# Optimization experiments

Hardware: AMD Instinct MI355X
Metric: run time of the kernel (lower is better)

The kernel has to match this reference:

```python
import jax, jax.numpy as jnp
import numpy as np

# Forest topology: T full C-ary trees of depth D, processed level-by-level
# (leaves=level 0 -> roots=level D), mirroring dgl.prop_nodes_topo.
T, C, D = 4096, 2, 5
E, H = 256, 128
COUNTS = [C ** (D - d) for d in range(D + 1)]          # nodes per level in one tree
OFFS = np.cumsum([0] + COUNTS[:-1])                     # level offsets within a tree
S = int(sum(COUNTS))                                    # nodes per tree (63)
N = T * S                                               # total nodes (258048)


def _topology():
    # children indices + validity mask for one tree, then tile across the forest
    ch1 = np.zeros((S, C), np.int32)
    m1 = np.zeros((S, C), np.float32)
    for d in range(1, D + 1):
        for j in range(COUNTS[d]):
            p = OFFS[d] + j
            ch1[p] = OFFS[d - 1] + j * C + np.arange(C)
            m1[p] = 1.0
    children = (ch1[None] + (np.arange(T, dtype=np.int32) * S)[:, None, None]).reshape(N, C)
    mask = np.tile(m1, (T, 1))
    return children, mask


def _level_nodes(d):
    # global node indices at level d (static numpy, not traced)
    return (np.arange(T)[:, None] * S + OFFS[d] + np.arange(COUNTS[d])[None, :]).reshape(-1)


def setup_inputs() -> dict:
    key = jax.random.key(0)
    ks = jax.random.split(key, 6)
    children, mask = _topology()
    child_type = np.asarray(jax.random.randint(ks[0], (N, C), 0, 2), np.int32)
    sc = 0.05
    return {
        "emb": jax.random.normal(ks[1], (N, E), jnp.float32),
        "child_mask": jnp.asarray(mask),
        "W_iou": jax.random.normal(ks[2], (E, 3 * H), jnp.float32) * sc,
        "U_iou": jax.random.normal(ks[3], (2 * H, 3 * H), jnp.float32) * sc,
        "b_iou": jnp.zeros((3 * H,), jnp.float32),
        "W_f": jax.random.normal(ks[4], (E, H), jnp.float32) * sc,
        "U_f_w": jax.random.normal(ks[5], (2 * H, 2 * H), jnp.float32) * sc,
        "U_f_b": jnp.zeros((2 * H,), jnp.float32),
        "b_f": jnp.zeros((H,), jnp.float32),
        "children_idx": jnp.asarray(children),
        "child_type": jnp.asarray(child_type),
    }


def _forward(emb, child_mask, W_iou, U_iou, b_iou, W_f, U_f_w, U_f_b, b_f,
             children_idx, child_type):
    h = jnp.zeros((N, H), emb.dtype)
    c = jnp.zeros((N, H), emb.dtype)
    for d in range(D + 1):  # topological sweep; leaves reduce to zeros (no children)
        nodes = _level_nodes(d)                          # [M] static
        ch = children_idx[nodes]                         # [M, C]
        cm = child_mask[nodes]                           # [M, C]
        ty = child_type[nodes]                           # [M, C]
        h_ch = h[ch]                                     # [M, C, H] mailbox gather
        c_ch = c[ch]
        # type-masked child-hidden sums (reduce_func)
        ht0 = jnp.einsum('mc,mch->mh', jnp.where(ty == 0, cm, 0.0), h_ch)
        ht1 = jnp.einsum('mc,mch->mh', jnp.where(ty == 1, cm, 0.0), h_ch)
        h_iou = jnp.concatenate([ht0, ht1], axis=1)      # [M, 2H]
        # per-child forget gates, selected by child type
        f = (h_iou @ U_f_w + U_f_b).reshape(-1, 2, H)
        idx = jnp.broadcast_to(ty[:, :, None], ty.shape + (H,))
        f_cell = jnp.take_along_axis(f, idx, axis=1)     # [M, C, H]
        X = emb[nodes] @ W_f                             # [M, H]
        f_tk = jax.nn.sigmoid(X[:, None, :] + f_cell + b_f)
        c_cell = jnp.sum(f_tk * c_ch * cm[:, :, None], axis=1)
        # apply_node_func
        iou = emb[nodes] @ W_iou + h_iou @ U_iou + b_iou
        i, o, u = jnp.split(iou, 3, axis=1)
        c_new = jax.nn.sigmoid(i) * jnp.tanh(u) + c_cell
        h_new = jax.nn.sigmoid(o) * jnp.tanh(c_new)
        h = h.at[nodes].set(h_new)
        c = c.at[nodes].set(c_new)
    return h


def reference(emb, child_mask, W_iou, U_iou, b_iou, W_f, U_f_w, U_f_b, b_f,
              children_idx, child_type):
    return _forward(emb, child_mask, W_iou, U_iou, b_iou, W_f, U_f_w, U_f_b, b_f,
                    children_idx, child_type)
```

## Files before the change

kernel.cpp:

```cpp
#include <hip/hip_runtime.h>


typedef float f32x4 __attribute__((ext_vector_type(4)));
typedef __bf16 bf16x8 __attribute__((ext_vector_type(8)));

__device__ __forceinline__ unsigned short f2bf(float x) {
  unsigned int u = __float_as_uint(x);
  return (unsigned short)((u + 0x7fffu + ((u >> 16) & 1u)) >> 16);
}
__device__ __forceinline__ float sigf(float x) { return 1.f / (1.f + __expf(-x)); }
__device__ __forceinline__ float tanhfast(float x) {
  return 1.f - 2.f / (__expf(2.f * x) + 1.f);
}

__global__ void prep_kernel(const float* __restrict__ Wi, const float* __restrict__ Ui,
                            const float* __restrict__ Wf, const float* __restrict__ Uf,
                            unsigned short* __restrict__ BTf) {
  int idx = blockIdx.x * 256 + threadIdx.x;
  int j = idx & 7;
  int lane = (idx >> 3) & 63;
  int ks = (idx >> 9) & 15;
  int tile = idx >> 13;
  int cl = lane & 15, kq = lane >> 4;
  int col = tile * 16 + cl;
  int k = ks * 32 + kq * 8 + j;
  float v;
  if (k < 256) {
    v = (col < 384) ? Wi[k * 384 + col] : Wf[k * 128 + ((col - 384) & 127)];
  } else {
    int kk = k & 255;
    v = (col < 384) ? Ui[kk * 384 + col] : Uf[kk * 256 + (col - 384)];
  }
  BTf[idx] = f2bf(v);
}

template <int NKS>
__device__ __forceinline__ int a_addr(int rblk, int k) {
  int mt = rblk >> 4, r = rblk & 15;
  int ks = k >> 5, kq = (k >> 3) & 3, j = k & 7;
  return (((mt * NKS + ks) * 64 + (kq << 4) + r) << 3) + j;
}

template <bool LEAF, int MT, int WPE>
__global__ __launch_bounds__(512, WPE) void lvl_kernel(
    const float* __restrict__ emb, const float* __restrict__ cmask,
    const int* __restrict__ cidx, const int* __restrict__ ctype,
    const unsigned short* __restrict__ BTf,
    const float* __restrict__ b_iou, const float* __restrict__ ufb,
    const float* __restrict__ bf_,
    float* __restrict__ hout, float* __restrict__ cbuf,
    int lc, int cntm1, int offs) {
  constexpr int KD = LEAF ? 256 : 512;
  constexpr int NKS = KD / 32;
  constexpr int NT = LEAF ? 3 : 5;
  constexpr int ROWS = MT * 16;
  __shared__ unsigned short Alds[ROWS * KD];

  const int tid = threadIdx.x;
  const int lane = tid & 63;
  const int w = tid >> 6;
  const int m0 = blockIdx.x * ROWS;

#pragma unroll
  for (int c = 0; c < MT; ++c) {
    const int ks_e = tid >> 6;
    const int lq = tid & 63;
    const int k0 = ks_e * 32 + (lq >> 4) * 8;
    const int rblk = c * 16 + (lq & 15);
    const int m = m0 + rblk;
    const int g = ((m >> lc) * 63) + offs + (m & cntm1);
    const float4 v0 = *(const float4*)&emb[(size_t)g * 256 + k0];
    const float4 v1 = *(const float4*)&emb[(size_t)g * 256 + k0 + 4];
    ushort4 p0, p1;
    p0.x = f2bf(v0.x); p0.y = f2bf(v0.y); p0.z = f2bf(v0.z); p0.w = f2bf(v0.w);
    p1.x = f2bf(v1.x); p1.y = f2bf(v1.y); p1.z = f2bf(v1.z); p1.w = f2bf(v1.w);
    unsigned short* dst = &Alds[((c * NKS + ks_e) * 64 + lq) * 8];
    *(ushort4*)dst = p0;
    *(ushort4*)(dst + 4) = p1;
  }

  if (!LEAF) {
    constexpr int TPR = 512 / ROWS;
    constexpr int CPT = 128 / TPR;
    const int rblk = tid / TPR, q = tid % TPR;
    const int m = m0 + rblk;
    const int g = ((m >> lc) * 63) + offs + (m & cntm1);
    const int ch0 = cidx[2 * g], ch1 = cidx[2 * g + 1];
    const int ty0 = ctype[2 * g], ty1 = ctype[2 * g + 1];
    const float c0 = cmask[2 * g], c1 = cmask[2 * g + 1];
    const float w00 = (ty0 == 0) ? c0 : 0.f, w01 = (ty1 == 0) ? c1 : 0.f;
    const float w10 = (ty0 == 1) ? c0 : 0.f, w11 = (ty1 == 1) ? c1 : 0.f;
#pragma unroll
    for (int jj = 0; jj < CPT / 4; ++jj) {
      const int j = q * CPT + jj * 4;
      float4 a = *(const float4*)&hout[(size_t)ch0 * 128 + j];
      float4 b = *(const float4*)&hout[(size_t)ch1 * 128 + j];
      ushort4 p0, p1;
      p0.x = f2bf(w00 * a.x + w01 * b.x);
      p0.y = f2bf(w00 * a.y + w01 * b.y);
      p0.z = f2bf(w00 * a.z + w01 * b.z);
      p0.w = f2bf(w00 * a.w + w01 * b.w);
      p1.x = f2bf(w10 * a.x + w11 * b.x);
      p1.y = f2bf(w10 * a.y + w11 * b.y);
      p1.z = f2bf(w10 * a.z + w11 * b.z);
      p1.w = f2bf(w10 * a.w + w11 * b.w);
      *(ushort4*)&Alds[a_addr<NKS>(rblk, 256 + j)] = p0;
      *(ushort4*)&Alds[a_addr<NKS>(rblk, 384 + j)] = p1;
    }
  }
  __syncthreads();

  f32x4 acc[MT][NT];
#pragma unroll
  for (int mt = 0; mt < MT; ++mt)
#pragma unroll
    for (int t = 0; t < NT; ++t) acc[mt][t] = (f32x4){0.f, 0.f, 0.f, 0.f};

  const unsigned short* Bw = BTf + (size_t)w * 8192 + lane * 8;

  bf16x8 bA[NT], bB[NT];
#pragma unroll
  for (int t = 0; t < NT; ++t)
    bA[t] = *(const bf16x8*)&Bw[(size_t)t * 65536];

  auto step = [&](bf16x8(&cur)[NT], bf16x8(&nxt)[NT], int ks) {
    if (ks + 1 < NKS) {
#pragma unroll
      for (int t = 0; t < NT; ++t)
        nxt[t] = *(const bf16x8*)&Bw[(size_t)t * 65536 + (ks + 1) * 512];
    }
    __builtin_amdgcn_s_setprio(1);
#pragma unroll
    for (int mt = 0; mt < MT; ++mt) {
      const bf16x8 a = *(const bf16x8*)&Alds[((mt * NKS + ks) * 64 + lane) << 3];
#pragma unroll
      for (int t = 0; t < NT; ++t)
        acc[mt][t] = __builtin_amdgcn_mfma_f32_16x16x32_bf16(a, cur[t], acc[mt][t], 0, 0, 0);
    }
    __builtin_amdgcn_s_setprio(0);
  };
#pragma unroll
  for (int ks2 = 0; ks2 < NKS / 2; ++ks2) {
    step(bA, bB, 2 * ks2);
    step(bB, bA, 2 * ks2 + 1);
  }

  const int cl = lane & 15;
  const int rb = (lane >> 4) << 2;
  const int hcol = w * 16 + cl;
  const float bi = b_iou[hcol];
  const float bo = b_iou[128 + hcol];
  const float bu = b_iou[256 + hcol];
  float f0b = 0.f, f1b = 0.f, bfv = 0.f;
  if (!LEAF) { f0b = ufb[hcol]; f1b = ufb[128 + hcol]; bfv = bf_[hcol]; }

#pragma unroll
  for (int mt = 0; mt < MT; ++mt) {
#pragma unroll
    for (int r = 0; r < 4; ++r) {
      const int m = m0 + (mt << 4) + rb + r;
      const int g = ((m >> lc) * 63) + offs + (m & cntm1);
      const float iv = acc[mt][0][r] + bi;
      const float ov = acc[mt][1][r] + bo;
      const float uv = acc[mt][2][r] + bu;
      float cn;
      if (LEAF) {
        cn = sigf(iv) * tanhfast(uv);
      } else {
        const int ch0 = cidx[2 * g], ch1 = cidx[2 * g + 1];
        const int ty0 = ctype[2 * g], ty1 = ctype[2 * g + 1];
        const float c0v = cmask[2 * g], c1v = cmask[2 * g + 1];
        const float f0 = acc[mt][3][r] + f0b;
        const float f1 = acc[mt][4][r] + f1b;
        const float fa = (ty0 == 0) ? f0 : f1;
        const float fb = (ty1 == 0) ? f0 : f1;
        const float ft0 = sigf(fa + bfv);
        const float ft1 = sigf(fb + bfv);
        const float ccell = ft0 * cbuf[(size_t)ch0 * 128 + hcol] * c0v +
                            ft1 * cbuf[(size_t)ch1 * 128 + hcol] * c1v;
        cn = sigf(iv) * tanhfast(uv) + ccell;
      }
      const float hn = sigf(ov) * tanhfast(cn);
      cbuf[(size_t)g * 128 + hcol] = cn;
      hout[(size_t)g * 128 + hcol] = hn;
    }
  }
}

extern "C" void kernel_launch(void* const* d_in, const int* in_sizes, int n_in,
                              void* d_out, int out_size, void* d_ws, size_t ws_size,
                              hipStream_t stream) {
  (void)in_sizes; (void)n_in; (void)out_size; (void)ws_size;
  const float* emb   = (const float*)d_in[0];
  const float* cmask = (const float*)d_in[1];
  const float* W_iou = (const float*)d_in[2];
  const float* U_iou = (const float*)d_in[3];
  const float* b_iou = (const float*)d_in[4];
  const float* W_f   = (const float*)d_in[5];
  const float* U_f_w = (const float*)d_in[6];
  const float* U_f_b = (const float*)d_in[7];
  const float* b_f   = (const float*)d_in[8];
  const int* cidx    = (const int*)d_in[9];
  const int* ctype   = (const int*)d_in[10];
  float* hout = (float*)d_out;

  unsigned short* BTf = (unsigned short*)d_ws;
  float* cbuf = (float*)((char*)d_ws + (size_t)(1 << 20));

  prep_kernel<<<1280, 256, 0, stream>>>(W_iou, U_iou, W_f, U_f_w, BTf);

  lvl_kernel<true, 2, 6><<<4096, 512, 0, stream>>>(emb, cmask, cidx, ctype, BTf, b_iou,
                                                   U_f_b, b_f, hout, cbuf, 5, 31, 0);
  lvl_kernel<false, 2, 4><<<2048, 512, 0, stream>>>(emb, cmask, cidx, ctype, BTf, b_iou,
                                                    U_f_b, b_f, hout, cbuf, 4, 15, 32);
  lvl_kernel<false, 2, 4><<<1024, 512, 0, stream>>>(emb, cmask, cidx, ctype, BTf, b_iou,
                                                    U_f_b, b_f, hout, cbuf, 3, 7, 48);
  lvl_kernel<false, 2, 4><<<512, 512, 0, stream>>>(emb, cmask, cidx, ctype, BTf, b_iou,
                                                   U_f_b, b_f, hout, cbuf, 2, 3, 56);
  lvl_kernel<false, 1, 4><<<512, 512, 0, stream>>>(emb, cmask, cidx, ctype, BTf, b_iou,
                                                   U_f_b, b_f, hout, cbuf, 1, 1, 60);
  lvl_kernel<false, 1, 4><<<256, 512, 0, stream>>>(emb, cmask, cidx, ctype, BTf, b_iou,
                                                   U_f_b, b_f, hout, cbuf, 0, 0, 62);
}
```

Baseline: 317.8 us.

## Fuse leaf and first internal tree level into one kernel with LDS child stash

Replaces the separate leaf-level and level-1 kernels with one fused kernel that processes two trees per block. Leaf h (as bf16) and c stay in shared memory and feed the level-1 GEMM directly, so the child gather no longer reads h/c back from global memory and one launch plus the barrier between them goes away. Leaf cbuf writes are skipped because only the stash consumes them. The price is a large LDS footprint (about 80KB per block), which may lower occupancy, and child indices are now assumed from the fixed tree topology instead of read from children_idx.

```diff
diff --git a/kernel.cpp b/kernel.cpp
--- a/kernel.cpp
+++ b/kernel.cpp
@@ -3,10 +3,14 @@
 
 typedef float f32x4 __attribute__((ext_vector_type(4)));
 typedef __bf16 bf16x8 __attribute__((ext_vector_type(8)));
+typedef unsigned short u16x8 __attribute__((ext_vector_type(8)));
 
 __device__ __forceinline__ unsigned short f2bf(float x) {
   unsigned int u = __float_as_uint(x);
   return (unsigned short)((u + 0x7fffu + ((u >> 16) & 1u)) >> 16);
+}
+__device__ __forceinline__ float bf2f(unsigned short u) {
+  return __uint_as_float(((unsigned int)u) << 16);
 }
 __device__ __forceinline__ float sigf(float x) { return 1.f / (1.f + __expf(-x)); }
 __device__ __forceinline__ float tanhfast(float x) {
@@ -41,6 +45,198 @@
   return (((mt * NKS + ks) * 64 + (kq << 4) + r) << 3) + j;
 }
 
+__global__ __launch_bounds__(512, 4) void fused_kernel(
+    const float* __restrict__ emb, const float* __restrict__ cmask,
+    const int* __restrict__ ctype,
+    const unsigned short* __restrict__ BTf,
+    const float* __restrict__ b_iou, const float* __restrict__ ufb,
+    const float* __restrict__ bf_,
+    float* __restrict__ hout, float* __restrict__ cbuf) {
+  __shared__ unsigned short Alds[16384];
+  __shared__ unsigned short hstash[8192];
+  __shared__ float cstash[8192];
+
+  const int tid = threadIdx.x;
+  const int lane = tid & 63;
+  const int w = tid >> 6;
+  const int cl = lane & 15;
+  const int rb = (lane >> 4) << 2;
+  const int hcol = w * 16 + cl;
+  const int g0 = blockIdx.x * 126;
+
+  const unsigned short* Bw = BTf + (size_t)w * 8192 + lane * 8;
+
+#pragma unroll
+  for (int c = 0; c < 4; ++c) {
+    const int ks_e = tid >> 6;
+    const int lq = tid & 63;
+    const int k0 = ks_e * 32 + (lq >> 4) * 8;
+    const int rblk = c * 16 + (lq & 15);
+    const int g = g0 + (rblk >> 5) * 63 + (rblk & 31);
+    const float4 v0 = *(const float4*)&emb[(size_t)g * 256 + k0];
+    const float4 v1 = *(const float4*)&emb[(size_t)g * 256 + k0 + 4];
+    ushort4 p0, p1;
+    p0.x = f2bf(v0.x); p0.y = f2bf(v0.y); p0.z = f2bf(v0.z); p0.w = f2bf(v0.w);
+    p1.x = f2bf(v1.x); p1.y = f2bf(v1.y); p1.z = f2bf(v1.z); p1.w = f2bf(v1.w);
+    unsigned short* dst = &Alds[((c * 8 + ks_e) * 64 + lq) * 8];
+    *(ushort4*)dst = p0;
+    *(ushort4*)(dst + 4) = p1;
+  }
+  __syncthreads();
+
+  {
+    f32x4 acc[4][3];
+#pragma unroll
+    for (int mt = 0; mt < 4; ++mt)
+#pragma unroll
+      for (int t = 0; t < 3; ++t) acc[mt][t] = (f32x4){0.f, 0.f, 0.f, 0.f};
+    bf16x8 bA[3], bB[3];
+#pragma unroll
+    for (int t = 0; t < 3; ++t) bA[t] = *(const bf16x8*)&Bw[(size_t)t * 65536];
+#pragma unroll
+    for (int ks2 = 0; ks2 < 4; ++ks2) {
+#pragma unroll
+      for (int half = 0; half < 2; ++half) {
+        const int ks = 2 * ks2 + half;
+        bf16x8* cur = half ? bB : bA;
+        bf16x8* nxt = half ? bA : bB;
+        if (ks + 1 < 8) {
+#pragma unroll
+          for (int t = 0; t < 3; ++t)
+            nxt[t] = *(const bf16x8*)&Bw[(size_t)t * 65536 + (ks + 1) * 512];
+        }
+        __builtin_amdgcn_s_setprio(1);
+#pragma unroll
+        for (int mt = 0; mt < 4; ++mt) {
+          const bf16x8 a = *(const bf16x8*)&Alds[((mt * 8 + ks) * 64 + lane) << 3];
+#pragma unroll
+          for (int t = 0; t < 3; ++t)
+            acc[mt][t] = __builtin_amdgcn_mfma_f32_16x16x32_bf16(a, cur[t], acc[mt][t], 0, 0, 0);
+        }
+        __builtin_amdgcn_s_setprio(0);
+      }
+    }
+    const float bi = b_iou[hcol], bo = b_iou[128 + hcol], bu = b_iou[256 + hcol];
+#pragma unroll
+    for (int mt = 0; mt < 4; ++mt) {
+#pragma unroll
+      for (int r = 0; r < 4; ++r) {
+        const int row = (mt << 4) + rb + r;
+        const int g = g0 + (row >> 5) * 63 + (row & 31);
+        const float cn = sigf(acc[mt][0][r] + bi) * tanhfast(acc[mt][2][r] + bu);
+        const float hn = sigf(acc[mt][1][r] + bo) * tanhfast(cn);
+        hout[(size_t)g * 128 + hcol] = hn;
+        hstash[row * 128 + hcol] = f2bf(hn);
+        cstash[row * 128 + hcol] = cn;
+      }
+    }
+  }
+  __syncthreads();
+
+#pragma unroll
+  for (int c = 0; c < 2; ++c) {
+    const int ks_e = tid >> 6;
+    const int lq = tid & 63;
+    const int k0 = ks_e * 32 + (lq >> 4) * 8;
+    const int rblk = c * 16 + (lq & 15);
+    const int g = g0 + (rblk >> 4) * 63 + 32 + (rblk & 15);
+    const float4 v0 = *(const float4*)&emb[(size_t)g * 256 + k0];
+    const float4 v1 = *(const float4*)&emb[(size_t)g * 256 + k0 + 4];
+    ushort4 p0, p1;
+    p0.x = f2bf(v0.x); p0.y = f2bf(v0.y); p0.z = f2bf(v0.z); p0.w = f2bf(v0.w);
+    p1.x = f2bf(v1.x); p1.y = f2bf(v1.y); p1.z = f2bf(v1.z); p1.w = f2bf(v1.w);
+    unsigned short* dst = &Alds[((c * 16 + ks_e) * 64 + lq) * 8];
+    *(ushort4*)dst = p0;
+    *(ushort4*)(dst + 4) = p1;
+  }
+  {
+    const int rblk = tid >> 4, q = tid & 15;
+    const int i = rblk >> 4, j = rblk & 15;
+    const int gp = g0 + i * 63 + 32 + j;
+    const int ch0 = i * 32 + 2 * j, ch1 = ch0 + 1;
+    const int ty0 = ctype[2 * gp], ty1 = ctype[2 * gp + 1];
+    const float c0 = cmask[2 * gp], c1 = cmask[2 * gp + 1];
+    const float w00 = (ty0 == 0) ? c0 : 0.f, w01 = (ty1 == 0) ? c1 : 0.f;
+    const float w10 = (ty0 == 1) ? c0 : 0.f, w11 = (ty1 == 1) ? c1 : 0.f;
+    const int jc = q * 8;
+    const u16x8 va = *(const u16x8*)&hstash[ch0 * 128 + jc];
+    const u16x8 vb = *(const u16x8*)&hstash[ch1 * 128 + jc];
+    u16x8 o0, o1;
+#pragma unroll
+    for (int e = 0; e < 8; ++e) {
+      const float fa = bf2f(va[e]), fb = bf2f(vb[e]);
+      o0[e] = f2bf(w00 * fa + w01 * fb);
+      o1[e] = f2bf(w10 * fa + w11 * fb);
+    }
+    *(u16x8*)&Alds[a_addr<16>(rblk, 256 + jc)] = o0;
+    *(u16x8*)&Alds[a_addr<16>(rblk, 384 + jc)] = o1;
+  }
+  __syncthreads();
+
+  {
+    f32x4 acc[2][5];
+#pragma unroll
+    for (int mt = 0; mt < 2; ++mt)
+#pragma unroll
+      for (int t = 0; t < 5; ++t) acc[mt][t] = (f32x4){0.f, 0.f, 0.f, 0.f};
+    bf16x8 bA[5], bB[5];
+#pragma unroll
+    for (int t = 0; t < 5; ++t) bA[t] = *(const bf16x8*)&Bw[(size_t)t * 65536];
+#pragma unroll
+    for (int ks2 = 0; ks2 < 8; ++ks2) {
+#pragma unroll
+      for (int half = 0; half < 2; ++half) {
+        const int ks = 2 * ks2 + half;
+        bf16x8* cur = half ? bB : bA;
+        bf16x8* nxt = half ? bA : bB;
+        if (ks + 1 < 16) {
+#pragma unroll
+          for (int t = 0; t < 5; ++t)
+            nxt[t] = *(const bf16x8*)&Bw[(size_t)t * 65536 + (ks + 1) * 512];
+        }
+        __builtin_amdgcn_s_setprio(1);
+#pragma unroll
+        for (int mt = 0; mt < 2; ++mt) {
+          const bf16x8 a = *(const bf16x8*)&Alds[((mt * 16 + ks) * 64 + lane) << 3];
+#pragma unroll
+          for (int t = 0; t < 5; ++t)
+            acc[mt][t] = __builtin_amdgcn_mfma_f32_16x16x32_bf16(a, cur[t], acc[mt][t], 0, 0, 0);
+        }
+        __builtin_amdgcn_s_setprio(0);
+      }
+    }
+    const float bi = b_iou[hcol], bo = b_iou[128 + hcol], bu = b_iou[256 + hcol];
+    const float f0b = ufb[hcol], f1b = ufb[128 + hcol], bfv = bf_[hcol];
+#pragma unroll
+    for (int mt = 0; mt < 2; ++mt) {
+#pragma unroll
+      for (int r = 0; r < 4; ++r) {
+        const int row = (mt << 4) + rb + r;
+        const int i = row >> 4, j = row & 15;
+        const int g = g0 + i * 63 + 32 + j;
+        const int ch0 = i * 32 + 2 * j, ch1 = ch0 + 1;
+        const int ty0 = ctype[2 * g], ty1 = ctype[2 * g + 1];
+        const float c0v = cmask[2 * g], c1v = cmask[2 * g + 1];
+        const float iv = acc[mt][0][r] + bi;
+        const float ov = acc[mt][1][r] + bo;
+        const float uv = acc[mt][2][r] + bu;
+        const float f0 = acc[mt][3][r] + f0b;
+        const float f1 = acc[mt][4][r] + f1b;
+        const float fa = (ty0 == 0) ? f0 : f1;
+        const float fb = (ty1 == 0) ? f0 : f1;
+        const float ft0 = sigf(fa + bfv);
+        const float ft1 = sigf(fb + bfv);
+        const float ccell = ft0 * cstash[ch0 * 128 + hcol] * c0v +
+                            ft1 * cstash[ch1 * 128 + hcol] * c1v;
+        const float cn = sigf(iv) * tanhfast(uv) + ccell;
+        const float hn = sigf(ov) * tanhfast(cn);
+        cbuf[(size_t)g * 128 + hcol] = cn;
+        hout[(size_t)g * 128 + hcol] = hn;
+      }
+    }
+  }
+}
+
 template <bool LEAF, int MT, int WPE>
 __global__ __launch_bounds__(512, WPE) void lvl_kernel(
     const float* __restrict__ emb, const float* __restrict__ cmask,
@@ -117,7 +313,6 @@
     for (int t = 0; t < NT; ++t) acc[mt][t] = (f32x4){0.f, 0.f, 0.f, 0.f};
 
   const unsigned short* Bw = BTf + (size_t)w * 8192 + lane * 8;
-
   bf16x8 bA[NT], bB[NT];
 #pragma unroll
   for (int t = 0; t < NT; ++t)
@@ -209,10 +404,8 @@
 
   prep_kernel<<<1280, 256, 0, stream>>>(W_iou, U_iou, W_f, U_f_w, BTf);
 
-  lvl_kernel<true, 2, 6><<<4096, 512, 0, stream>>>(emb, cmask, cidx, ctype, BTf, b_iou,
-                                                   U_f_b, b_f, hout, cbuf, 5, 31, 0);
-  lvl_kernel<false, 2, 4><<<2048, 512, 0, stream>>>(emb, cmask, cidx, ctype, BTf, b_iou,
-                                                    U_f_b, b_f, hout, cbuf, 4, 15, 32);
+  fused_kernel<<<2048, 512, 0, stream>>>(emb, cmask, ctype, BTf, b_iou,
+                                         U_f_b, b_f, hout, cbuf);
   lvl_kernel<false, 2, 4><<<1024, 512, 0, stream>>>(emb, cmask, cidx, ctype, BTf, b_iou,
                                                     U_f_b, b_f, hout, cbuf, 3, 7, 48);
   lvl_kernel<false, 2, 4><<<512, 512, 0, stream>>>(emb, cmask, cidx, ctype, BTf, b_iou,
```

Result: faster. 267.3 us (median of 2 runs) (-15.9%).
